# Kernel optimization log

Measured on AMD Instinct MI355X. Metric: run time of the kernel, lower is better.

The kernel has to match this reference:

```python
import jax, jax.numpy as jnp
import numpy as np

B, S, D = 8, 1024, 128
EPS = 1e-7
LN_EPS = 1e-3  # keras LayerNormalization default


def setup_inputs() -> dict:
    key = jax.random.key(0)
    ks = jax.random.split(key, 8)
    sd = 1.0 / np.sqrt(D)
    return {
        "x": jax.random.normal(ks[0], (B, S, D), jnp.float32),
        "Wq": jax.random.normal(ks[1], (D, D), jnp.float32) * sd,
        "bq": jnp.zeros((D,), jnp.float32),
        "Wm": jax.random.normal(ks[2], (D, D), jnp.float32) * sd,
        "bm": jnp.zeros((D,), jnp.float32),
        "Ww": jax.random.normal(ks[3], (D, 1), jnp.float32) * sd,
        "bw": jnp.zeros((1,), jnp.float32),
        "Wc": jax.random.normal(ks[4], (D, 1), jnp.float32) * sd,
        "bc": jnp.zeros((1,), jnp.float32),
        "emb_map": jax.random.normal(ks[5], (D, D, D), jnp.float32) * 0.02,
        "gamma": jnp.ones((D,), jnp.float32),
        "beta": jnp.zeros((D,), jnp.float32),
    }


def reference(x, Wq, bq, Wm, bm, Ww, bw, Wc, bc, emb_map, gamma, beta):
    b_, s_, d_ = x.shape
    q = x @ Wq + bq                      # [B,S,D]
    m = jax.nn.sigmoid(x @ Wm + bm)      # [B,S,D]
    w = jax.nn.relu(x @ Ww + bw)         # [B,S,1]
    c = jax.nn.relu(x @ Wc + bc)         # [B,S,1]

    # distances: for query pos i, preceding pos j (j<i) has distance i-j
    idx = jnp.arange(s_)
    dist = (idx[:, None] - idx[None, :]).astype(x.dtype)   # [S,S]
    valid = dist > 0                                       # strict causal
    # cosh positional decay, zero outside causal window -> [B,S,S]
    pe = jnp.where(valid[None], 1.0 / jnp.cosh((dist[None] - c) / (w + EPS)), 0.0)

    # angle between (pe * x_j * m_i + eps) and (q_i + eps), expanded analytically
    qp = q + EPS
    t1 = jnp.einsum('bjd,bid->bij', x, m * qp)             # sum_d x_j m_i q'_i
    s1 = jnp.einsum('bjd,bid->bij', x, m)                  # sum_d x_j m_i
    s2 = jnp.einsum('bjd,bid->bij', x * x, m * m)          # sum_d (x_j m_i)^2
    dot = pe * t1 + EPS * jnp.sum(qp, axis=-1)[:, :, None]
    na = jnp.sqrt(pe * pe * s2 + 2.0 * EPS * pe * s1 + d_ * EPS * EPS)
    nb = jnp.linalg.norm(qp, axis=-1)[:, :, None]
    cos = jnp.where(valid[None], dot / (na * nb), 0.0)
    angle = jnp.where(valid[None], jnp.arccos(cos), 0.0)   # [B,S,S]

    # query_result_i = sum_j pe*angle * x_j  -> [B,S,D]
    qr = jnp.einsum('bij,bjd->bid', pe * angle, x)

    # embedding matrix: current_token (rows) outer query_result (cols),
    # contracted against rank-3 map: out[b,s,d] = sum_{j,k} x[b,s,j] qr[b,s,k] map[d,j,k]
    em = jnp.einsum('bsj,bsk->bsjk', x, qr).reshape(b_, s_, d_ * d_)
    mapped = em @ emb_map.reshape(d_, d_ * d_).T           # [B,S,D]

    res = mapped + x
    mu = jnp.mean(res, axis=-1, keepdims=True)
    var = jnp.var(res, axis=-1, keepdims=True)
    out = (res - mu) / jnp.sqrt(var + LN_EPS) * gamma + beta
    return out  # dropout is identity at inference
```

## Files before the change

### kernel.cpp

```cpp
#include <hip/hip_runtime.h>
#include <hip/hip_bf16.h>
#include <math.h>

#define DD 128
#define SS 1024
#define NROWS 8192
#define EPSF 1e-7f
#define LN_EPSF 1e-3f
#define TCUT 30.0f

typedef __attribute__((ext_vector_type(8))) short bf16x8;
typedef __attribute__((ext_vector_type(4))) float f32x4;
typedef __attribute__((ext_vector_type(16))) float f32x16;

__device__ __forceinline__ void gload_lds16(const void* g, void* l) {
    __builtin_amdgcn_global_load_lds(
        (const __attribute__((address_space(1))) unsigned int*)g,
        (__attribute__((address_space(3))) unsigned int*)l, 16, 0, 0);
}
__device__ __forceinline__ short f2bf(float v) {
    union { __hip_bfloat16 h; short s; } u;
    u.h = __float2bfloat16(v);
    return u.s;
}
__device__ __forceinline__ float bf2f(short s) {
    union { __hip_bfloat16 h; short s; } u; u.s = s;
    return __bfloat162float(u.h);
}
__device__ __forceinline__ unsigned int pack_bf16(float lo, float hi) {
    unsigned int r;
    asm("v_cvt_pk_bf16_f32 %0, %1, %2" : "=v"(r) : "v"(lo), "v"(hi));
    return r;
}
__device__ __forceinline__ float u2f(unsigned int u) {
    union { unsigned int u; float f; } c; c.u = u; return c.f;
}

__global__ __launch_bounds__(256) void k0a_emb(const float* __restrict__ emb,
                                               short* __restrict__ embh3) {
    __shared__ float lt[32][128];
    int d = blockIdx.x, js = blockIdx.y, t = threadIdx.x;
    {
        int jl = t >> 3, k0 = (t & 7) * 16;
        const float4* src = (const float4*)(emb + (size_t)d * 16384
                                            + (size_t)(js * 32 + jl) * 128 + k0);
#pragma unroll
        for (int q = 0; q < 4; ++q) *(float4*)&lt[jl][k0 + q * 4] = src[q];
    }
    __syncthreads();
    int ks = t >> 5, l0 = (t & 31) * 2;
    union { bf16x8 v[2]; short s[16]; } ob;
#pragma unroll
    for (int li = 0; li < 2; ++li) {
        int l = l0 + li;
        const float* p = &lt[l & 31][ks * 16 + (l >> 5) * 8];
#pragma unroll
        for (int e = 0; e < 8; ++e) ob.s[li * 8 + e] = f2bf(p[e]);
    }
    short* dst = embh3 + (size_t)(d * 4 + js) * 4096 + (size_t)t * 16;
    *(bf16x8*)dst = ob.v[0];
    *(bf16x8*)(dst + 8) = ob.v[1];
}

__global__ __launch_bounds__(256) void k0w_split(const float* __restrict__ Wq,
        const float* __restrict__ Wm, short* __restrict__ Wfrag) {
    int T = blockIdx.x * 256 + threadIdx.x;
    int e = T & 7, l = (T >> 3) & 63, ks = (T >> 9) & 3, nt = (T >> 11) & 7,
        mat = (T >> 14) & 1;
    int k = ks * 32 + ((l >> 4) & 3) * 8 + e;
    int c = nt * 16 + (l & 15);
    float v = (mat ? Wm : Wq)[k * 128 + c];
    short h = f2bf(v);
    float lo = v - bf2f(h);
    Wfrag[((((size_t)(mat * 2 + 0) * 8 + nt) * 4 + ks) * 64 + l) * 8 + e] = h;
    Wfrag[((((size_t)(mat * 2 + 1) * 8 + nt) * 4 + ks) * 64 + l) * 8 + e] = f2bf(lo);
}

__global__ __launch_bounds__(256) void k0c_xsplit(const float* __restrict__ x,
        const float* __restrict__ Ww, const float* __restrict__ bw,
        const float* __restrict__ Wc, const float* __restrict__ bc,
        short* __restrict__ xh2, short* __restrict__ xl2,
        float* __restrict__ scal) {
    __shared__ float xs[32][129];
    int rb = blockIdx.x, t = threadIdx.x;
    {
        int r = t >> 3, d0 = (t & 7) * 16;
        const float4* src = (const float4*)(x + (size_t)(rb * 32 + r) * 128 + d0);
#pragma unroll
        for (int q = 0; q < 4; ++q) *(float4*)&xs[r][d0 + q * 4] = src[q];
    }
    __syncthreads();
    int ks = (t >> 5) & 3, rf = t >> 7, l0 = (t & 31) * 2;
    union { bf16x8 v[2]; short s[16]; } hb, lb;
#pragma unroll
    for (int li = 0; li < 2; ++li) {
        int l = l0 + li;
        const float* p = &xs[rf * 16 + (l & 15)][ks * 32 + ((l >> 4) & 3) * 8];
#pragma unroll
        for (int e = 0; e < 8; ++e) {
            float v = p[e];
            short h = f2bf(v);
            hb.s[li * 8 + e] = h;
            lb.s[li * 8 + e] = f2bf(v - bf2f(h));
        }
    }
    {
        short* d1 = xh2 + (size_t)rb * 4096 + (size_t)t * 16;
        short* d2 = xl2 + (size_t)rb * 4096 + (size_t)t * 16;
        *(bf16x8*)d1 = hb.v[0]; *(bf16x8*)(d1 + 8) = hb.v[1];
        *(bf16x8*)d2 = lb.v[0]; *(bf16x8*)(d2 + 8) = lb.v[1];
    }
    int rr = t >> 3, seg = t & 7;
    float pw = 0.f, pc = 0.f;
#pragma unroll
    for (int dq = 0; dq < 16; ++dq) {
        float xv = xs[rr][seg * 16 + dq];
        pw = fmaf(xv, Ww[seg * 16 + dq], pw);
        pc = fmaf(xv, Wc[seg * 16 + dq], pc);
    }
    pw += __shfl_xor(pw, 1); pw += __shfl_xor(pw, 2); pw += __shfl_xor(pw, 4);
    pc += __shfl_xor(pc, 1); pc += __shfl_xor(pc, 2); pc += __shfl_xor(pc, 4);
    if (seg == 0) {
        scal[(size_t)(rb * 32 + rr) * 4 + 0] = fmaxf(pw + bw[0], 0.f);
        scal[(size_t)(rb * 32 + rr) * 4 + 1] = fmaxf(pc + bc[0], 0.f);
    }
}

__global__ __launch_bounds__(256) void k1_mfma(
    const short* __restrict__ xh2, const short* __restrict__ xl2,
    const short* __restrict__ Wfrag,
    const float* __restrict__ bq, const float* __restrict__ bm,
    float* __restrict__ mq, float* __restrict__ mo, float* __restrict__ scal)
{
    __shared__ __align__(16) short wl[65536];
    __shared__ float red[32][4][2];
    int t = threadIdx.x, w = t >> 6, l = t & 63;
    int l15 = l & 15, g = l >> 4;
    int row0 = blockIdx.x * 32;
#pragma unroll
    for (int it = 0; it < 32; ++it)
        gload_lds16(Wfrag + (size_t)(it * 256 + t) * 8, wl + (size_t)(it * 256 + w * 64) * 8);
    const short* xb  = xh2 + (size_t)blockIdx.x * 4096;
    const short* xlb = xl2 + (size_t)blockIdx.x * 4096;
    bf16x8 Ah[2][4], Al[2][4];
#pragma unroll
    for (int rf = 0; rf < 2; ++rf)
#pragma unroll
        for (int ks = 0; ks < 4; ++ks) {
            size_t o = ((size_t)(rf * 4 + ks) * 64 + l) * 8;
            Ah[rf][ks] = *(const bf16x8*)(xb + o);
            Al[rf][ks] = *(const bf16x8*)(xlb + o);
        }
    __syncthreads();
    f32x4 accq[2][2] = {}, accm[2][2] = {};
#pragma unroll
    for (int ntp = 0; ntp < 2; ++ntp) {
        int nt = w * 2 + ntp;
#pragma unroll
        for (int ks = 0; ks < 4; ++ks) {
            bf16x8 bhq = *(const bf16x8*)(wl + ((size_t)(0  + nt) * 4 + ks) * 512 + l * 8);
            bf16x8 blq = *(const bf16x8*)(wl + ((size_t)(8  + nt) * 4 + ks) * 512 + l * 8);
            bf16x8 bhm = *(const bf16x8*)(wl + ((size_t)(16 + nt) * 4 + ks) * 512 + l * 8);
            bf16x8 blm = *(const bf16x8*)(wl + ((size_t)(24 + nt) * 4 + ks) * 512 + l * 8);
#pragma unroll
            for (int rf = 0; rf < 2; ++rf) {
                accq[rf][ntp] = __builtin_amdgcn_mfma_f32_16x16x32_bf16(Ah[rf][ks], bhq, accq[rf][ntp], 0, 0, 0);
                accq[rf][ntp] = __builtin_amdgcn_mfma_f32_16x16x32_bf16(Ah[rf][ks], blq, accq[rf][ntp], 0, 0, 0);
                accq[rf][ntp] = __builtin_amdgcn_mfma_f32_16x16x32_bf16(Al[rf][ks], bhq, accq[rf][ntp], 0, 0, 0);
                accm[rf][ntp] = __builtin_amdgcn_mfma_f32_16x16x32_bf16(Ah[rf][ks], bhm, accm[rf][ntp], 0, 0, 0);
                accm[rf][ntp] = __builtin_amdgcn_mfma_f32_16x16x32_bf16(Ah[rf][ks], blm, accm[rf][ntp], 0, 0, 0);
                accm[rf][ntp] = __builtin_amdgcn_mfma_f32_16x16x32_bf16(Al[rf][ks], bhm, accm[rf][ntp], 0, 0, 0);
            }
        }
    }
    float sq1[2][4] = {{0,0,0,0},{0,0,0,0}};
    float sq2[2][4] = {{0,0,0,0},{0,0,0,0}};
#pragma unroll
    for (int ntp = 0; ntp < 2; ++ntp) {
        int c = (w * 2 + ntp) * 16 + l15;
        float bqv = bq[c] + EPSF, bmv = bm[c];
#pragma unroll
        for (int rf = 0; rf < 2; ++rf)
#pragma unroll
            for (int reg = 0; reg < 4; ++reg) {
                int rloc = rf * 16 + g * 4 + reg;
                float qp = accq[rf][ntp][reg] + bqv;
                float mv = 1.0f / (1.0f + expf(-(accm[rf][ntp][reg] + bmv)));
                size_t o = (size_t)(row0 + rloc) * 128 + c;
                mq[o] = mv * qp;
                mo[o] = mv;
                sq1[rf][reg] += qp;
                sq2[rf][reg] += qp * qp;
            }
    }
#pragma unroll
    for (int rf = 0; rf < 2; ++rf)
#pragma unroll
        for (int reg = 0; reg < 4; ++reg) {
            float a = sq1[rf][reg], b = sq2[rf][reg];
            a += __shfl_xor(a, 1); a += __shfl_xor(a, 2);
            a += __shfl_xor(a, 4); a += __shfl_xor(a, 8);
            b += __shfl_xor(b, 1); b += __shfl_xor(b, 2);
            b += __shfl_xor(b, 4); b += __shfl_xor(b, 8);
            if (l15 == 0) {
                red[rf * 16 + g * 4 + reg][w][0] = a;
                red[rf * 16 + g * 4 + reg][w][1] = b;
            }
        }
    __syncthreads();
    if (t < 32) {
        float a = red[t][0][0] + red[t][1][0] + red[t][2][0] + red[t][3][0];
        float b = red[t][0][1] + red[t][1][1] + red[t][2][1] + red[t][3][1];
        scal[(size_t)(row0 + t) * 4 + 2] = a;
        scal[(size_t)(row0 + t) * 4 + 3] = sqrtf(b);
    }
}

__global__ __launch_bounds__(256) void k2_qr(
    const float* __restrict__ x,
    const float* __restrict__ mq, const float* __restrict__ mo,
    const float* __restrict__ scal, short* __restrict__ qrh2)
{
    int row = blockIdx.x;
    int i = row & (SS - 1);
    const float* xb = x + (size_t)(row - i) * DD;
    int t = threadIdx.x, w = t >> 6, l = t & 63;
    int sub = l >> 4, q = l & 15;
    int qo = q * 8;

    float mqv[8], mov[8];
    {
        const float* mp = mq + (size_t)row * DD + qo;
        float4 a = *(const float4*)mp, b = *(const float4*)(mp + 4);
        mqv[0] = a.x; mqv[1] = a.y; mqv[2] = a.z; mqv[3] = a.w;
        mqv[4] = b.x; mqv[5] = b.y; mqv[6] = b.z; mqv[7] = b.w;
        const float* op = mo + (size_t)row * DD + qo;
        float4 c = *(const float4*)op, d = *(const float4*)(op + 4);
        mov[0] = c.x; mov[1] = c.y; mov[2] = c.z; mov[3] = c.w;
        mov[4] = d.x; mov[5] = d.y; mov[6] = d.z; mov[7] = d.w;
    }
    float wv = scal[row * 4 + 0], cv = scal[row * 4 + 1];
    float sumqp = scal[row * 4 + 2], nb = scal[row * 4 + 3];
    float wi = wv + EPSF;
    float dmaxf = cv + TCUT * wi;
    int dmax = (dmaxf >= (float)i) ? i : (int)dmaxf;

    float acc[8] = {0.f, 0.f, 0.f, 0.f, 0.f, 0.f, 0.f, 0.f};
    int nit = (dmax + 15) >> 4;
    int dbase = 1 + w * 4 + sub;
    for (int it = 0; it < nit; ++it) {
        int dist = dbase + it * 16;
        float xv[8];
        if (dist <= dmax) {
            const float* xp = xb + (size_t)(i - dist) * DD + qo;
            float4 a = *(const float4*)xp, b = *(const float4*)(xp + 4);
            xv[0] = a.x; xv[1] = a.y; xv[2] = a.z; xv[3] = a.w;
            xv[4] = b.x; xv[5] = b.y; xv[6] = b.z; xv[7] = b.w;
        } else {
#pragma unroll
            for (int e = 0; e < 8; ++e) xv[e] = 0.f;
        }
        float t1 = 0.f, s1 = 0.f, s2 = 0.f;
#pragma unroll
        for (int e = 0; e < 8; ++e) {
            float xm = xv[e] * mov[e];
            t1 = fmaf(xv[e], mqv[e], t1);
            s1 += xm;
            s2 = fmaf(xm, xm, s2);
        }
#pragma unroll
        for (int off = 1; off < 16; off <<= 1) {
            t1 += __shfl_xor(t1, off);
            s1 += __shfl_xor(s1, off);
            s2 += __shfl_xor(s2, off);
        }
        float tt = ((float)dist - cv) / wi;
        float pe = 1.0f / coshf(tt);
        float dotv = fmaf(pe, t1, EPSF * sumqp);
        float na = sqrtf(fmaf(pe * pe, s2,
                         fmaf(2.0f * EPSF * pe, s1, (float)DD * EPSF * EPSF)));
        float cosv = fminf(1.0f, fmaxf(-1.0f, dotv / (na * nb)));
        float ang = acosf(cosv);
        float wgt = pe * ang;
#pragma unroll
        for (int e = 0; e < 8; ++e) acc[e] = fmaf(wgt, xv[e], acc[e]);
    }
#pragma unroll
    for (int e = 0; e < 8; ++e) {
        acc[e] += __shfl_xor(acc[e], 16);
        acc[e] += __shfl_xor(acc[e], 32);
    }
    __shared__ float sq[4][DD];
    if (l < 16) {
#pragma unroll
        for (int e = 0; e < 8; ++e) sq[w][qo + e] = acc[e];
    }
    __syncthreads();
    if (t < DD) {
        float v = sq[0][t] + sq[1][t] + sq[2][t] + sq[3][t];
        int rbq = row >> 7, rr = row & 127, rt2 = rr >> 5, lp = rr & 31;
        int k = t;
        qrh2[(((size_t)(rbq * 4 + rt2) * 8 + (k >> 4)) * 64
              + (lp + 32 * ((k >> 3) & 1))) * 8 + (k & 7)] = f2bf(v);
    }
}

__global__ __launch_bounds__(512, 2) void k3_gemm(
    const float* __restrict__ x, const short* __restrict__ embh3,
    const short* __restrict__ qrh2, short* __restrict__ partb)
{
    __shared__ __align__(16) char ldsb[81920];
    short* xtwh = (short*)ldsb;
    short* elds = (short*)ldsb;
    short* swb  = (short*)(ldsb + 65536);

    int t = threadIdx.x, w8 = t >> 6, l = t & 63;
    int l31 = l & 31, hi = l >> 5;
    int kp = w8 & 1, rh = w8 >> 1;
    int rc = blockIdx.x, dq = blockIdx.y, js = blockIdx.z;

#pragma unroll
    for (int i = 0; i < 8; ++i) {
        int idx = i * 512 + t;
        int r = idx >> 3, j4 = (idx & 7) * 4;
        float4 v = *(const float4*)(x + (size_t)(rc * 512 + r) * 128 + js * 32 + j4);
        *(unsigned int*)(xtwh + r * 36 + j4)     = pack_bf16(v.x, v.y);
        *(unsigned int*)(xtwh + r * 36 + j4 + 2) = pack_bf16(v.z, v.w);
    }

    bf16x8 Bf[4][4];
    int rbq = rc * 4 + rh;
#pragma unroll
    for (int rt = 0; rt < 4; ++rt)
#pragma unroll
        for (int s = 0; s < 4; ++s)
            Bf[rt][s] = *(const bf16x8*)(qrh2
                + (((size_t)(rbq * 4 + rt) * 8 + kp * 4 + s) * 64 + l) * 8);

    __syncthreads();

    float xv[4][16];
#pragma unroll
    for (int rt = 0; rt < 4; ++rt) {
        int row_l = rh * 128 + rt * 32 + l31;
#pragma unroll
        for (int p = 0; p < 8; ++p) {
            int jA = ((2 * p) & 3) + 8 * (p >> 1) + 4 * hi;
            unsigned int u = *(const unsigned int*)(xtwh + row_l * 36 + jA);
            xv[rt][2 * p]     = u2f(u << 16);
            xv[rt][2 * p + 1] = u2f(u & 0xFFFF0000u);
        }
    }

    __syncthreads();

#pragma unroll
    for (int i = 0; i < 8; ++i) {
        int c = i * 512 + t;
        int d = c >> 9, off = c & 511;
        gload_lds16(embh3 + (size_t)((dq * 8 + d) * 4 + js) * 4096 + (size_t)off * 8,
                    elds + (size_t)(i * 512 + w8 * 64) * 8);
    }
    __syncthreads();

    float sprev[4];
    short* swbase = swb + (kp * 512 + rh * 128 + l31) * 8;

#define K3_DSTEP(DI, ODD)                                                    \
    {                                                                        \
        bf16x8 A[4];                                                         \
        _Pragma("unroll")                                                    \
        for (int s = 0; s < 4; ++s)                                          \
            A[s] = *(const bf16x8*)(elds + (DI) * 4096                       \
                                    + ((kp * 4 + s) * 64 + l) * 8);          \
        _Pragma("unroll")                                                    \
        for (int rtp = 0; rtp < 2; ++rtp) {                                  \
            f32x16 ac0, ac1;                                                 \
            _Pragma("unroll")                                                \
            for (int q = 0; q < 16; ++q) { ac0[q] = 0.f; ac1[q] = 0.f; }     \
            _Pragma("unroll")                                                \
            for (int s = 0; s < 4; ++s) {                                    \
                ac0 = __builtin_amdgcn_mfma_f32_32x32x16_bf16(               \
                    A[s], Bf[rtp * 2][s], ac0, 0, 0, 0);                     \
                ac1 = __builtin_amdgcn_mfma_f32_32x32x16_bf16(               \
                    A[s], Bf[rtp * 2 + 1][s], ac1, 0, 0, 0);                 \
            }                                                                \
            float sm0 = 0.f, sm1 = 0.f;                                      \
            _Pragma("unroll")                                                \
            for (int q = 0; q < 16; ++q) {                                   \
                sm0 = fmaf(xv[rtp * 2][q], ac0[q], sm0);                     \
                sm1 = fmaf(xv[rtp * 2 + 1][q], ac1[q], sm1);                 \
            }                                                                \
            sm0 += __shfl_xor(sm0, 32);                                      \
            sm1 += __shfl_xor(sm1, 32);                                      \
            if (ODD) {                                                       \
                if (hi == 0) {                                               \
                    *(unsigned int*)(swbase + rtp * 2 * 32 * 8 + (DI) - 1)   \
                        = pack_bf16(sprev[rtp * 2], sm0);                    \
                    *(unsigned int*)(swbase + (rtp * 2 + 1) * 32 * 8 + (DI) - 1) \
                        = pack_bf16(sprev[rtp * 2 + 1], sm1);                \
                }                                                            \
            } else {                                                         \
                sprev[rtp * 2] = sm0;                                        \
                sprev[rtp * 2 + 1] = sm1;                                    \
            }                                                                \
        }                                                                    \
    }

#pragma unroll
    for (int dp = 0; dp < 4; ++dp) {
        K3_DSTEP(2 * dp, 0)
        K3_DSTEP(2 * dp + 1, 1)
    }
#undef K3_DSTEP

    __syncthreads();
#pragma unroll
    for (int i = 0; i < 2; ++i) {
        int c = i * 512 + t;
        int kp2 = c >> 9, rl = c & 511;
        *(bf16x8*)(partb + (size_t)(js * 2 + kp2) * 1048576
                   + (size_t)(rc * 512 + rl) * 128 + dq * 8)
            = *(const bf16x8*)(swb + (kp2 * 512 + rl) * 8);
    }
}

__global__ __launch_bounds__(256) void k4_ln(
    const float* __restrict__ x, const short* __restrict__ partb,
    const float* __restrict__ gamma, const float* __restrict__ beta,
    float* __restrict__ out)
{
    int wave = threadIdx.x >> 6, lane = threadIdx.x & 63;
    int row = blockIdx.x * 4 + wave;
    size_t base = (size_t)row * DD;
    float r0 = x[base + lane], r1 = x[base + lane + 64];
#pragma unroll
    for (int p = 0; p < 8; ++p) {
        r0 += bf2f(partb[(size_t)p * 1048576 + base + lane]);
        r1 += bf2f(partb[(size_t)p * 1048576 + base + lane + 64]);
    }
    float s = r0 + r1, s2 = r0 * r0 + r1 * r1;
#pragma unroll
    for (int off = 32; off > 0; off >>= 1) {
        s += __shfl_xor(s, off);
        s2 += __shfl_xor(s2, off);
    }
    float mu = s * (1.0f / DD);
    float var = s2 * (1.0f / DD) - mu * mu;
    var = fmaxf(var, 0.0f);
    float rs = rsqrtf(var + LN_EPSF);
    out[base + lane] = (r0 - mu) * rs * gamma[lane] + beta[lane];
    out[base + lane + 64] = (r1 - mu) * rs * gamma[lane + 64] + beta[lane + 64];
}

extern "C" void kernel_launch(void* const* d_in, const int* in_sizes, int n_in,
                              void* d_out, int out_size, void* d_ws, size_t ws_size,
                              hipStream_t stream) {
    const float* x     = (const float*)d_in[0];
    const float* Wq    = (const float*)d_in[1];
    const float* bq    = (const float*)d_in[2];
    const float* Wm    = (const float*)d_in[3];
    const float* bm    = (const float*)d_in[4];
    const float* Ww    = (const float*)d_in[5];
    const float* bw    = (const float*)d_in[6];
    const float* Wc    = (const float*)d_in[7];
    const float* bc    = (const float*)d_in[8];
    const float* emb   = (const float*)d_in[9];
    const float* gamma = (const float*)d_in[10];
    const float* beta  = (const float*)d_in[11];
    float* out = (float*)d_out;
    float* ws  = (float*)d_ws;

    short* embh3 = (short*)ws;
    short* qrh2  = (short*)(ws + 1048576);
    float* scal  = ws + 1572864;
    short* partb = (short*)(ws + 1605632);
    float* tr    = ws + 1605632;
    short* xh2   = (short*)tr;
    short* xl2   = (short*)(tr + 524288);
    float* mq    = tr + 1048576;
    float* mo    = tr + 2097152;
    short* Wfrag = (short*)(tr + 3145728);

    hipLaunchKernelGGL(k0a_emb,   dim3(128, 4), dim3(256), 0, stream, emb, embh3);
    hipLaunchKernelGGL(k0w_split, dim3(256),    dim3(256), 0, stream, Wq, Wm, Wfrag);
    hipLaunchKernelGGL(k0c_xsplit,dim3(256),    dim3(256), 0, stream,
                       x, Ww, bw, Wc, bc, xh2, xl2, scal);
    hipLaunchKernelGGL(k1_mfma,   dim3(256),    dim3(256), 0, stream,
                       xh2, xl2, Wfrag, bq, bm, mq, mo, scal);
    hipLaunchKernelGGL(k2_qr,     dim3(8192),   dim3(256), 0, stream,
                       x, mq, mo, scal, qrh2);
    hipLaunchKernelGGL(k3_gemm,   dim3(16, 16, 4), dim3(512), 0, stream,
                       x, embh3, qrh2, partb);
    hipLaunchKernelGGL(k4_ln,     dim3(2048),   dim3(256), 0, stream,
                       x, partb, gamma, beta, out);
}
```

Baseline: 92.98 us.

## Restructure k3 GEMM to full-K per wave and fp32 partials

```diff
diff --git a/kernel.cpp b/kernel.cpp
--- a/kernel.cpp
+++ b/kernel.cpp
@@ -305,44 +305,44 @@
     }
 }
 
-__global__ __launch_bounds__(512, 2) void k3_gemm(
+__global__ __launch_bounds__(256, 2) void k3_gemm(
     const float* __restrict__ x, const short* __restrict__ embh3,
-    const short* __restrict__ qrh2, short* __restrict__ partb)
+    const short* __restrict__ qrh2, float* __restrict__ part)
 {
-    __shared__ __align__(16) char ldsb[81920];
+    __shared__ __align__(16) char ldsb[65536];
     short* xtwh = (short*)ldsb;
     short* elds = (short*)ldsb;
-    short* swb  = (short*)(ldsb + 65536);
-
-    int t = threadIdx.x, w8 = t >> 6, l = t & 63;
+    float* sof  = (float*)ldsb;
+
+    int t = threadIdx.x, w = t >> 6, l = t & 63;
     int l31 = l & 31, hi = l >> 5;
-    int kp = w8 & 1, rh = w8 >> 1;
     int rc = blockIdx.x, dq = blockIdx.y, js = blockIdx.z;
 
 #pragma unroll
     for (int i = 0; i < 8; ++i) {
-        int idx = i * 512 + t;
+        int idx = i * 256 + t;
         int r = idx >> 3, j4 = (idx & 7) * 4;
-        float4 v = *(const float4*)(x + (size_t)(rc * 512 + r) * 128 + js * 32 + j4);
+        float4 v = *(const float4*)(x + (size_t)(rc * 256 + r) * 128 + js * 32 + j4);
         *(unsigned int*)(xtwh + r * 36 + j4)     = pack_bf16(v.x, v.y);
         *(unsigned int*)(xtwh + r * 36 + j4 + 2) = pack_bf16(v.z, v.w);
     }
 
-    bf16x8 Bf[4][4];
-    int rbq = rc * 4 + rh;
-#pragma unroll
-    for (int rt = 0; rt < 4; ++rt)
-#pragma unroll
-        for (int s = 0; s < 4; ++s)
+    bf16x8 Bf[2][8];
+#pragma unroll
+    for (int rt = 0; rt < 2; ++rt) {
+        int R32 = rc * 8 + w * 2 + rt;
+#pragma unroll
+        for (int s = 0; s < 8; ++s)
             Bf[rt][s] = *(const bf16x8*)(qrh2
-                + (((size_t)(rbq * 4 + rt) * 8 + kp * 4 + s) * 64 + l) * 8);
-
-    __syncthreads();
-
-    float xv[4][16];
-#pragma unroll
-    for (int rt = 0; rt < 4; ++rt) {
-        int row_l = rh * 128 + rt * 32 + l31;
+                + (((size_t)R32 * 8 + s) * 64 + l) * 8);
+    }
+
+    __syncthreads();
+
+    float xv[2][16];
+#pragma unroll
+    for (int rt = 0; rt < 2; ++rt) {
+        int row_l = w * 64 + rt * 32 + l31;
 #pragma unroll
         for (int p = 0; p < 8; ++p) {
             int jA = ((2 * p) & 3) + 8 * (p >> 1) + 4 * hi;
@@ -355,78 +355,67 @@
     __syncthreads();
 
 #pragma unroll
-    for (int i = 0; i < 8; ++i) {
-        int c = i * 512 + t;
+    for (int i = 0; i < 16; ++i) {
+        int c = i * 256 + t;
         int d = c >> 9, off = c & 511;
         gload_lds16(embh3 + (size_t)((dq * 8 + d) * 4 + js) * 4096 + (size_t)off * 8,
-                    elds + (size_t)(i * 512 + w8 * 64) * 8);
-    }
-    __syncthreads();
-
-    float sprev[4];
-    short* swbase = swb + (kp * 512 + rh * 128 + l31) * 8;
-
-#define K3_DSTEP(DI, ODD)                                                    \
-    {                                                                        \
-        bf16x8 A[4];                                                         \
-        _Pragma("unroll")                                                    \
-        for (int s = 0; s < 4; ++s)                                          \
-            A[s] = *(const bf16x8*)(elds + (DI) * 4096                       \
-                                    + ((kp * 4 + s) * 64 + l) * 8);          \
-        _Pragma("unroll")                                                    \
-        for (int rtp = 0; rtp < 2; ++rtp) {                                  \
-            f32x16 ac0, ac1;                                                 \
-            _Pragma("unroll")                                                \
-            for (int q = 0; q < 16; ++q) { ac0[q] = 0.f; ac1[q] = 0.f; }     \
-            _Pragma("unroll")                                                \
-            for (int s = 0; s < 4; ++s) {                                    \
-                ac0 = __builtin_amdgcn_mfma_f32_32x32x16_bf16(               \
-                    A[s], Bf[rtp * 2][s], ac0, 0, 0, 0);                     \
-                ac1 = __builtin_amdgcn_mfma_f32_32x32x16_bf16(               \
-                    A[s], Bf[rtp * 2 + 1][s], ac1, 0, 0, 0);                 \
-            }                                                                \
-            float sm0 = 0.f, sm1 = 0.f;                                      \
-            _Pragma("unroll")                                                \
-            for (int q = 0; q < 16; ++q) {                                   \
-                sm0 = fmaf(xv[rtp * 2][q], ac0[q], sm0);                     \
-                sm1 = fmaf(xv[rtp * 2 + 1][q], ac1[q], sm1);                 \
-            }                                                                \
-            sm0 += __shfl_xor(sm0, 32);                                      \
-            sm1 += __shfl_xor(sm1, 32);                                      \
-            if (ODD) {                                                       \
-                if (hi == 0) {                                               \
-                    *(unsigned int*)(swbase + rtp * 2 * 32 * 8 + (DI) - 1)   \
-                        = pack_bf16(sprev[rtp * 2], sm0);                    \
-                    *(unsigned int*)(swbase + (rtp * 2 + 1) * 32 * 8 + (DI) - 1) \
-                        = pack_bf16(sprev[rtp * 2 + 1], sm1);                \
-                }                                                            \
-            } else {                                                         \
-                sprev[rtp * 2] = sm0;                                        \
-                sprev[rtp * 2 + 1] = sm1;                                    \
-            }                                                                \
-        }                                                                    \
-    }
-
-#pragma unroll
-    for (int dp = 0; dp < 4; ++dp) {
-        K3_DSTEP(2 * dp, 0)
-        K3_DSTEP(2 * dp + 1, 1)
-    }
-#undef K3_DSTEP
-
-    __syncthreads();
+                    elds + (size_t)(i * 256 + w * 64) * 8);
+    }
+    __syncthreads();
+
+    float sout[2][8];
+
+#pragma unroll
+    for (int d = 0; d < 8; ++d) {
+        bf16x8 A[8];
+#pragma unroll
+        for (int s = 0; s < 8; ++s)
+            A[s] = *(const bf16x8*)(elds + d * 4096 + (s * 64 + l) * 8);
+#pragma unroll
+        for (int rt = 0; rt < 2; ++rt) {
+            f32x16 acc;
+#pragma unroll
+            for (int q = 0; q < 16; ++q) acc[q] = 0.f;
+#pragma unroll
+            for (int s = 0; s < 8; ++s)
+                acc = __builtin_amdgcn_mfma_f32_32x32x16_bf16(A[s], Bf[rt][s],
+                                                              acc, 0, 0, 0);
+            float s0 = 0.f, s1 = 0.f, s2 = 0.f, s3 = 0.f;
+#pragma unroll
+            for (int q = 0; q < 4; ++q) {
+                s0 = fmaf(xv[rt][q * 4 + 0], acc[q * 4 + 0], s0);
+                s1 = fmaf(xv[rt][q * 4 + 1], acc[q * 4 + 1], s1);
+                s2 = fmaf(xv[rt][q * 4 + 2], acc[q * 4 + 2], s2);
+                s3 = fmaf(xv[rt][q * 4 + 3], acc[q * 4 + 3], s3);
+            }
+            float sm = (s0 + s1) + (s2 + s3);
+            sm += __shfl_xor(sm, 32);
+            sout[rt][d] = sm;
+        }
+    }
+
+    __syncthreads();
+    if (hi == 0) {
+#pragma unroll
+        for (int rt = 0; rt < 2; ++rt)
+#pragma unroll
+            for (int d = 0; d < 8; ++d)
+                sof[(w * 64 + rt * 32 + l31) * 8 + d] = sout[rt][d];
+    }
+    __syncthreads();
+
 #pragma unroll
     for (int i = 0; i < 2; ++i) {
-        int c = i * 512 + t;
-        int kp2 = c >> 9, rl = c & 511;
-        *(bf16x8*)(partb + (size_t)(js * 2 + kp2) * 1048576
-                   + (size_t)(rc * 512 + rl) * 128 + dq * 8)
-            = *(const bf16x8*)(swb + (kp2 * 512 + rl) * 8);
+        int idx = i * 256 + t;
+        int r = idx >> 1, q = (idx & 1) * 4;
+        float4 v = *(const float4*)&sof[r * 8 + q];
+        *(float4*)(part + (size_t)js * (NROWS * DD)
+                   + (size_t)(rc * 256 + r) * 128 + dq * 8 + q) = v;
     }
 }
 
 __global__ __launch_bounds__(256) void k4_ln(
-    const float* __restrict__ x, const short* __restrict__ partb,
+    const float* __restrict__ x, const float* __restrict__ part,
     const float* __restrict__ gamma, const float* __restrict__ beta,
     float* __restrict__ out)
 {
@@ -435,9 +424,9 @@
     size_t base = (size_t)row * DD;
     float r0 = x[base + lane], r1 = x[base + lane + 64];
 #pragma unroll
-    for (int p = 0; p < 8; ++p) {
-        r0 += bf2f(partb[(size_t)p * 1048576 + base + lane]);
-        r1 += bf2f(partb[(size_t)p * 1048576 + base + lane + 64]);
+    for (int p = 0; p < 4; ++p) {
+        r0 += part[(size_t)p * NROWS * DD + base + lane];
+        r1 += part[(size_t)p * NROWS * DD + base + lane + 64];
     }
     float s = r0 + r1, s2 = r0 * r0 + r1 * r1;
 #pragma unroll
@@ -474,7 +463,7 @@
     short* embh3 = (short*)ws;
     short* qrh2  = (short*)(ws + 1048576);
     float* scal  = ws + 1572864;
-    short* partb = (short*)(ws + 1605632);
+    float* part  = ws + 1605632;
     float* tr    = ws + 1605632;
     short* xh2   = (short*)tr;
     short* xl2   = (short*)(tr + 524288);
@@ -490,8 +479,8 @@
                        xh2, xl2, Wfrag, bq, bm, mq, mo, scal);
     hipLaunchKernelGGL(k2_qr,     dim3(8192),   dim3(256), 0, stream,
                        x, mq, mo, scal, qrh2);
-    hipLaunchKernelGGL(k3_gemm,   dim3(16, 16, 4), dim3(512), 0, stream,
-                       x, embh3, qrh2, partb);
+    hipLaunchKernelGGL(k3_gemm,   dim3(32, 16, 4), dim3(256), 0, stream,
+                       x, embh3, qrh2, part);
     hipLaunchKernelGGL(k4_ln,     dim3(2048),   dim3(256), 0, stream,
-                       x, partb, gamma, beta, out);
-}
+                       x, part, gamma, beta, out);
+}
```

Measured after the change: 90.87 us. 2.3% less time.
